# Optimization experiments

Hardware: AMD Instinct MI355X
Metric: run time of the kernel (lower is better)

Reference implementation:

```python
import jax, jax.numpy as jnp
import numpy as np

D_MODEL, D_FF, N_EXPERTS, TOP_K = 1024, 4096, 8, 2
B, S = 4, 4096


def setup_inputs() -> dict:
    key = jax.random.key(0)
    ks = jax.random.split(key, 4)
    scale_in = 1.0 / np.sqrt(D_MODEL)
    scale_ff = 1.0 / np.sqrt(D_FF)
    return {
        "x": jax.random.normal(ks[0], (B, S, D_MODEL), dtype=jnp.float32),
        "gate_w": jax.random.normal(ks[1], (D_MODEL, N_EXPERTS), dtype=jnp.float32) * scale_in,
        "gate_b": jnp.zeros((N_EXPERTS,), dtype=jnp.float32),
        "w1": jax.random.normal(ks[2], (N_EXPERTS, D_MODEL, D_FF), dtype=jnp.float32) * scale_in,
        "b1": jnp.zeros((N_EXPERTS, D_FF), dtype=jnp.float32),
        "w2": jax.random.normal(ks[3], (N_EXPERTS, D_FF, D_MODEL), dtype=jnp.float32) * scale_ff,
        "b2": jnp.zeros((N_EXPERTS, D_MODEL), dtype=jnp.float32),
    }


def reference(x, gate_w, gate_b, w1, b1, w2, b2):
    in_shape = x.shape
    tokens = x.reshape(-1, in_shape[-1])                      # [T, d]
    logits = tokens @ gate_w + gate_b                         # [T, E]
    top_w, sel = jax.lax.top_k(logits, TOP_K)                 # [T, k]
    top_w = jax.nn.softmax(top_w.astype(jnp.float32), axis=1).astype(tokens.dtype)

    out = jnp.zeros_like(tokens)
    for e in range(N_EXPERTS):
        # combined routing weight for expert e (0 if not selected) -> [T]
        coef = jnp.sum(jnp.where(sel == e, top_w, 0.0), axis=1)
        h = jax.nn.silu(tokens @ w1[e] + b1[e])               # [T, d_ff]
        y = h @ w2[e] + b2[e]                                 # [T, d]
        out = out + coef[:, None] * y
    return out.reshape(in_shape)
```

## Files before the change

kernel.cpp:

```cpp
#include <hip/hip_runtime.h>
#include <hip/hip_bf16.h>
#include <stdint.h>

#define DM 1024
#define DF 4096
#define NE 8
#define TT 16384
#define MAXTILES 144
#define CAP (MAXTILES * 256)

typedef __bf16 bf16;
typedef __attribute__((ext_vector_type(8))) __bf16 bf16x8;
typedef __attribute__((ext_vector_type(4))) __bf16 bf16x4;
typedef __attribute__((ext_vector_type(4))) float f32x4;

#define AS1 __attribute__((address_space(1)))
#define AS3 __attribute__((address_space(3)))

__device__ __forceinline__ void async16(void* lds, const void* g) {
  __builtin_amdgcn_global_load_lds((const AS1 uint32_t*)g, (AS3 uint32_t*)lds, 16, 0, 0);
}

__global__ void k_gate(const float* __restrict__ x, const float* __restrict__ gw,
                       const float* __restrict__ gb,
                       int* __restrict__ sel, float* __restrict__ cw) {
  int gid = blockIdx.x * blockDim.x + threadIdx.x;
  int tok = gid >> 6;
  int lane = threadIdx.x & 63;
  const float* xr = x + (size_t)tok * DM;
  float l[8] = {0,0,0,0,0,0,0,0};
#pragma unroll
  for (int i = 0; i < DM / 64; i++) {
    int d = i * 64 + lane;
    float xv = xr[d];
    float4 gA = *(const float4*)(gw + d * 8);
    float4 gB = *(const float4*)(gw + d * 8 + 4);
    l[0] += xv * gA.x; l[1] += xv * gA.y; l[2] += xv * gA.z; l[3] += xv * gA.w;
    l[4] += xv * gB.x; l[5] += xv * gB.y; l[6] += xv * gB.z; l[7] += xv * gB.w;
  }
#pragma unroll
  for (int e = 0; e < 8; e++) {
    float v = l[e];
    v += __shfl_xor(v, 1);  v += __shfl_xor(v, 2);  v += __shfl_xor(v, 4);
    v += __shfl_xor(v, 8);  v += __shfl_xor(v, 16); v += __shfl_xor(v, 32);
    l[e] = v + gb[e];
  }
  if (lane == 0) {
    int e0 = 0;
#pragma unroll
    for (int e = 1; e < 8; e++) if (l[e] > l[e0]) e0 = e;
    int e1 = (e0 == 0) ? 1 : 0;
#pragma unroll
    for (int e = 0; e < 8; e++) if (e != e1 && e != e0 && l[e] > l[e1]) e1 = e;
    float t = expf(l[e1] - l[e0]);
    float c0 = 1.0f / (1.0f + t);
    float c1 = t / (1.0f + t);
    sel[2 * tok] = e0;  sel[2 * tok + 1] = e1;
    cw[2 * tok] = c0;   cw[2 * tok + 1] = c1;
  }
}

__global__ void k_hist(const int* __restrict__ sel, int* __restrict__ meta) {
  __shared__ int h[8];
  if (threadIdx.x < 8) h[threadIdx.x] = 0;
  __syncthreads();
  int i = blockIdx.x * blockDim.x + threadIdx.x;
  atomicAdd(&h[sel[i]], 1);
  __syncthreads();
  if (threadIdx.x < 8) atomicAdd(&meta[threadIdx.x], h[threadIdx.x]);
}

__global__ void k_plan(int* __restrict__ meta, int* __restrict__ rows) {
  if (threadIdx.x == 0) {
    int off = 0, nt = 0;
    for (int e = 0; e < NE; e++) {
      meta[16 + e] = off;
      int c = meta[e];
      int ntile = (c + 255) >> 8;
      for (int j = 0; j < ntile; j++) {
        meta[64 + nt] = e;
        meta[64 + MAXTILES + nt] = off + j * 256;
        nt++;
      }
      off += ntile * 256;
    }
    meta[24] = nt;
    meta[25] = off;
  }
  __syncthreads();
  for (int i = threadIdx.x; i < CAP; i += blockDim.x) rows[i] = -1;
}

__global__ void k_scatter(const int* __restrict__ sel, const float* __restrict__ cw,
                          int* __restrict__ meta, int* __restrict__ rows,
                          float* __restrict__ coefs) {
  __shared__ int hcnt[8];
  __shared__ int hbase[8];
  if (threadIdx.x < 8) hcnt[threadIdx.x] = 0;
  __syncthreads();
  int slot = blockIdx.x * 256 + threadIdx.x;
  int t = slot >> 1;
  int e = sel[slot];
  int r = atomicAdd(&hcnt[e], 1);
  __syncthreads();
  if (threadIdx.x < 8) hbase[threadIdx.x] = atomicAdd(&meta[8 + threadIdx.x], hcnt[threadIdx.x]);
  __syncthreads();
  int pos = meta[16 + e] + hbase[e] + r;
  rows[pos] = t;
  coefs[pos] = cw[slot];
}

__global__ void k_gather(const float* __restrict__ x, const int* __restrict__ rows,
                         const int* __restrict__ meta, bf16* __restrict__ xg) {
  int pos = blockIdx.x;
  if (pos >= meta[25]) return;
  int t = rows[pos];
  int c = threadIdx.x * 4;
  bf16x4 o;
  if (t >= 0) {
    float4 f = *(const float4*)(x + (size_t)t * DM + c);
    o[0] = (bf16)f.x; o[1] = (bf16)f.y; o[2] = (bf16)f.z; o[3] = (bf16)f.w;
  } else {
    o[0] = (bf16)0.0f; o[1] = (bf16)0.0f; o[2] = (bf16)0.0f; o[3] = (bf16)0.0f;
  }
  *(bf16x4*)(xg + (size_t)pos * DM + c) = o;
}

__global__ void k_transcast(const float* __restrict__ src, bf16* __restrict__ dst,
                            int srcRS, size_t srcE, size_t dstE, int R) {
  __shared__ float tile[64][65];
  src += blockIdx.z * srcE;
  dst += blockIdx.z * dstE;
  int r0 = blockIdx.y * 64, c0 = blockIdx.x * 64;
  int tr = threadIdx.x >> 4;
  int tc = (threadIdx.x & 15) * 4;
#pragma unroll
  for (int i = 0; i < 4; i++) {
    int r = tr + i * 16;
    float4 f = *(const float4*)(src + (size_t)(r0 + r) * srcRS + (c0 + tc));
    tile[r][tc] = f.x; tile[r][tc + 1] = f.y; tile[r][tc + 2] = f.z; tile[r][tc + 3] = f.w;
  }
  __syncthreads();
#pragma unroll
  for (int i = 0; i < 4; i++) {
    int cc = tr + i * 16;
    bf16x4 o;
    o[0] = (bf16)tile[tc + 0][cc];
    o[1] = (bf16)tile[tc + 1][cc];
    o[2] = (bf16)tile[tc + 2][cc];
    o[3] = (bf16)tile[tc + 3][cc];
    *(bf16x4*)(dst + (size_t)(c0 + cc) * R + (r0 + tc)) = o;
  }
}

template<int MODE>
__global__ __launch_bounds__(512, 1) void k_gemm(
    const bf16* __restrict__ A, const bf16* __restrict__ Bw,
    const float* __restrict__ bias, int bstride,
    bf16* __restrict__ H, float* __restrict__ Out, int addBias,
    const int* __restrict__ rows, const float* __restrict__ coefs,
    const int* __restrict__ meta, int KT, int NT) {
  int T = meta[24];
  int ngx = NT >> 8;
  int nact = ngx * T;
  int b = blockIdx.x;
  if (b >= nact) return;
  int q = nact >> 3, rr = nact & 7;
  int xcd = b & 7, i = b >> 3;
  int j = xcd * q + (xcd < rr ? xcd : rr) + i;
  int gT4 = T << 2;
  int g = j / gT4;
  int rem = j - g * gT4;
  int tidb = rem >> 2;
  int xnb = (g << 2) + (rem & 3);
  int e = meta[64 + tidb];
  int row0 = meta[64 + MAXTILES + tidb];
  int n0 = xnb << 8;

  __shared__ __align__(16) bf16 As[2][256 * 64];
  __shared__ __align__(16) bf16 Bs[2][256 * 64];

  int t = threadIdx.x;
  int lane = t & 63;
  int w = t >> 6;
  int wm = w >> 2, wn = w & 3;

  int arow = t >> 3;
  int k8 = ((t & 7) ^ (arow & 7)) * 8;
  const bf16* Ab = A + (size_t)(row0 + arow) * KT + k8;
  const bf16* Bb = Bw + ((size_t)e * NT + n0 + arow) * KT + k8;
  size_t rstep = (size_t)64 * KT;
  int ldso = t * 8;

  f32x4 acc[8][4] = {};

  auto stage_B_A02 = [&](int kt, int buf) {
    const bf16* a = Ab + kt;
    const bf16* b2 = Bb + kt;
    bf16* la = &As[buf][ldso];
    bf16* lb = &Bs[buf][ldso];
    async16(lb,         b2);
    async16(lb + 4096,  b2 + rstep);
    async16(lb + 8192,  b2 + 2 * rstep);
    async16(lb + 12288, b2 + 3 * rstep);
    async16(la,         a);
    async16(la + 8192,  a + 2 * rstep);
  };
  auto stage_A13 = [&](int kt, int buf) {
    const bf16* a = Ab + kt;
    bf16* la = &As[buf][ldso];
    async16(la + 4096,  a + rstep);
    async16(la + 12288, a + 3 * rstep);
  };

  int rA = (wm * 128 + (lane & 15)) * 64;
  int rB = (wn * 64 + (lane & 15)) * 64;
  int kx0 = ((lane >> 4) * 8) ^ ((lane & 7) * 8);
  int kx1 = kx0 ^ 32;

  int nt = KT >> 6;
  stage_B_A02(0, 0);
  stage_A13(0, 0);
  stage_B_A02(64, 1);
  asm volatile("s_waitcnt vmcnt(8)" ::: "memory");
  __builtin_amdgcn_s_barrier();

  bf16x8 bfr[2][4];
  for (int tau = 0; tau < nt; ++tau) {
    int s = tau & 1;
    const bf16* Ap = &As[s][rA];
    const bf16* Bp = &Bs[s][rB];
    {
      bf16x8 af[2][4];
#pragma unroll
      for (int ni = 0; ni < 4; ni++) {
        bfr[0][ni] = *(const bf16x8*)&Bp[ni * 1024 + kx0];
        bfr[1][ni] = *(const bf16x8*)&Bp[ni * 1024 + kx1];
      }
#pragma unroll
      for (int mi = 0; mi < 4; mi++) {
        af[0][mi] = *(const bf16x8*)&Ap[mi * 1024 + kx0];
        af[1][mi] = *(const bf16x8*)&Ap[mi * 1024 + kx1];
      }
      if (tau + 1 < nt) stage_A13((tau + 1) << 6, s ^ 1);
      __builtin_amdgcn_s_setprio(1);
#pragma unroll
      for (int ks = 0; ks < 2; ks++)
#pragma unroll
        for (int mi = 0; mi < 4; mi++)
#pragma unroll
          for (int ni = 0; ni < 4; ni++)
            acc[mi][ni] = __builtin_amdgcn_mfma_f32_16x16x32_bf16(
                af[ks][mi], bfr[ks][ni], acc[mi][ni], 0, 0, 0);
      __builtin_amdgcn_s_setprio(0);
    }
    if (tau < nt - 1) asm volatile("s_waitcnt vmcnt(8)" ::: "memory");
    else              asm volatile("s_waitcnt vmcnt(0)" ::: "memory");
    __builtin_amdgcn_s_barrier();
    {
      bf16x8 af[2][4];
#pragma unroll
      for (int mi = 0; mi < 4; mi++) {
        af[0][mi] = *(const bf16x8*)&Ap[(mi + 4) * 1024 + kx0];
        af[1][mi] = *(const bf16x8*)&Ap[(mi + 4) * 1024 + kx1];
      }
      if (tau + 2 < nt) stage_B_A02((tau + 2) << 6, s);
      __builtin_amdgcn_s_setprio(1);
#pragma unroll
      for (int ks = 0; ks < 2; ks++)
#pragma unroll
        for (int mi = 0; mi < 4; mi++)
#pragma unroll
          for (int ni = 0; ni < 4; ni++)
            acc[mi + 4][ni] = __builtin_amdgcn_mfma_f32_16x16x32_bf16(
                af[ks][mi], bfr[ks][ni], acc[mi + 4][ni], 0, 0, 0);
      __builtin_amdgcn_s_setprio(0);
    }
    if (tau < nt - 2)       asm volatile("s_waitcnt vmcnt(8)" ::: "memory");
    else if (tau == nt - 2) asm volatile("s_waitcnt vmcnt(2)" ::: "memory");
    else                    asm volatile("s_waitcnt vmcnt(0)" ::: "memory");
    __builtin_amdgcn_s_barrier();
  }

  int rq = (lane >> 4) * 4;
  int cq = lane & 15;
  float bv[4];
#pragma unroll
  for (int ni = 0; ni < 4; ni++)
    bv[ni] = bias[e * bstride + n0 + wn * 64 + ni * 16 + cq];

  if (MODE == 0) {
#pragma unroll
    for (int mi = 0; mi < 8; mi++) {
#pragma unroll
      for (int i2 = 0; i2 < 4; i2++) {
        int gr = row0 + wm * 128 + mi * 16 + rq + i2;
        bf16* hr = H + (size_t)gr * NT + n0 + wn * 64;
#pragma unroll
        for (int ni = 0; ni < 4; ni++) {
          float v = acc[mi][ni][i2] + bv[ni];
          float sg = v / (1.0f + __expf(-v));
          hr[ni * 16 + cq] = (bf16)sg;
        }
      }
    }
  } else {
#pragma unroll
    for (int mi = 0; mi < 8; mi++) {
#pragma unroll
      for (int i2 = 0; i2 < 4; i2++) {
        int gr = row0 + wm * 128 + mi * 16 + rq + i2;
        int trow = rows[gr];
        if (trow < 0) continue;
        float cf = coefs[gr];
        float* orow = Out + (size_t)trow * DM + n0 + wn * 64;
#pragma unroll
        for (int ni = 0; ni < 4; ni++) {
          float v = acc[mi][ni][i2];
          if (addBias) v += bv[ni];
          atomicAdd(&orow[ni * 16 + cq], cf * v);
        }
      }
    }
  }
}

extern "C" void kernel_launch(void* const* d_in, const int* in_sizes, int n_in,
                              void* d_out, int out_size, void* d_ws, size_t ws_size,
                              hipStream_t stream) {
  const float* x  = (const float*)d_in[0];
  const float* gw = (const float*)d_in[1];
  const float* gb = (const float*)d_in[2];
  const float* w1 = (const float*)d_in[3];
  const float* b1 = (const float*)d_in[4];
  const float* w2 = (const float*)d_in[5];
  const float* b2 = (const float*)d_in[6];
  float* out = (float*)d_out;

  size_t smallB = (size_t)CAP * 4 * 2 + (size_t)TT * 2 * 4 * 2 + 8192 + 16 * 256;
  int nc = 8;
  for (int cand = 1; cand <= 8; cand <<= 1) {
    size_t dfc = DF / cand;
    size_t need = 2 * ((size_t)NE * dfc * DM * 2)
                + (size_t)CAP * DM * 2
                + (size_t)CAP * dfc * 2
                + smallB;
    if (need <= ws_size) { nc = cand; break; }
  }
  const int DFC = DF / nc;

  char* ws = (char*)d_ws;
  size_t off = 0;
  auto alloc = [&](size_t bytes) -> void* {
    void* p = ws + off;
    off += (bytes + 255) & ~(size_t)255;
    return p;
  };
  bf16* w1tc = (bf16*)alloc((size_t)NE * DFC * DM * 2);
  bf16* w2tc = (bf16*)alloc((size_t)NE * DM * DFC * 2);
  bf16* xg   = (bf16*)alloc((size_t)CAP * DM * 2);
  bf16* h    = (bf16*)alloc((size_t)CAP * DFC * 2);
  int* rows  = (int*)alloc((size_t)CAP * 4);
  float* cof = (float*)alloc((size_t)CAP * 4);
  int* sel   = (int*)alloc((size_t)TT * 2 * 4);
  float* cw  = (float*)alloc((size_t)TT * 2 * 4);
  int* meta  = (int*)alloc(8192);

  hipMemsetAsync(meta, 0, 256, stream);
  hipMemsetAsync(out, 0, (size_t)out_size * sizeof(float), stream);
  k_gate<<<TT / 4, 256, 0, stream>>>(x, gw, gb, sel, cw);
  k_hist<<<2 * TT / 256, 256, 0, stream>>>(sel, meta);
  k_plan<<<1, 256, 0, stream>>>(meta, rows);
  k_scatter<<<2 * TT / 256, 256, 0, stream>>>(sel, cw, meta, rows, cof);
  k_gather<<<CAP, 256, 0, stream>>>(x, rows, meta, xg);

  for (int c = 0; c < nc; c++) {
    const float* w1c = w1 + (size_t)c * DFC;
    const float* w2c = w2 + (size_t)c * DFC * DM;
    k_transcast<<<dim3(DFC / 64, DM / 64, NE), 256, 0, stream>>>(
        w1c, w1tc, DF, (size_t)DM * DF, (size_t)DFC * DM, DM);
    k_transcast<<<dim3(DM / 64, DFC / 64, NE), 256, 0, stream>>>(
        w2c, w2tc, DM, (size_t)DF * DM, (size_t)DM * DFC, DFC);
    k_gemm<0><<<(DFC / 256) * MAXTILES, 512, 0, stream>>>(
        xg, w1tc, b1 + (size_t)c * DFC, DF, h, nullptr, 0, rows, cof, meta, DM, DFC);
    k_gemm<1><<<(DM / 256) * MAXTILES, 512, 0, stream>>>(
        h, w2tc, b2, DM, nullptr, out, (c == 0) ? 1 : 0, rows, cof, meta, DFC, DM);
  }
}
```

Before: 955.1 us.

## Split each GEMM K-tile half into two phases with interleaved async loads

The main loop of the expert GEMM now processes each half of the 64-wide K tile in two 32-wide sub-phases separated by extra barriers. The global-to-LDS async loads for the next tiles are spread across these four phases instead of issued in two bursts. Only half of the fragments are held live at a time, which lowers register pressure. The goal is to smooth memory issue against MFMA work, at the cost of two extra workgroup barriers per iteration.

```diff
diff --git a/kernel.cpp b/kernel.cpp
--- a/kernel.cpp
+++ b/kernel.cpp
@@ -194,34 +194,25 @@
 
   f32x4 acc[8][4] = {};
 
-  auto stage_B_A02 = [&](int kt, int buf) {
-    const bf16* a = Ab + kt;
-    const bf16* b2 = Bb + kt;
-    bf16* la = &As[buf][ldso];
-    bf16* lb = &Bs[buf][ldso];
-    async16(lb,         b2);
-    async16(lb + 4096,  b2 + rstep);
-    async16(lb + 8192,  b2 + 2 * rstep);
-    async16(lb + 12288, b2 + 3 * rstep);
-    async16(la,         a);
-    async16(la + 8192,  a + 2 * rstep);
-  };
-  auto stage_A13 = [&](int kt, int buf) {
-    const bf16* a = Ab + kt;
-    bf16* la = &As[buf][ldso];
-    async16(la + 4096,  a + rstep);
-    async16(la + 12288, a + 3 * rstep);
-  };
-
   int rA = (wm * 128 + (lane & 15)) * 64;
   int rB = (wn * 64 + (lane & 15)) * 64;
   int kx0 = ((lane >> 4) * 8) ^ ((lane & 7) * 8);
   int kx1 = kx0 ^ 32;
 
   int nt = KT >> 6;
-  stage_B_A02(0, 0);
-  stage_A13(0, 0);
-  stage_B_A02(64, 1);
+  {
+    const bf16* a0 = Ab;  const bf16* b0 = Bb;
+    bf16* la = &As[0][ldso];  bf16* lb = &Bs[0][ldso];
+    async16(lb, b0); async16(lb + 4096, b0 + rstep);
+    async16(lb + 8192, b0 + 2 * rstep); async16(lb + 12288, b0 + 3 * rstep);
+    async16(la, a0); async16(la + 8192, a0 + 2 * rstep);
+    async16(la + 4096, a0 + rstep); async16(la + 12288, a0 + 3 * rstep);
+    const bf16* a1 = Ab + 64;  const bf16* b1 = Bb + 64;
+    bf16* la1 = &As[1][ldso];  bf16* lb1 = &Bs[1][ldso];
+    async16(lb1, b1); async16(lb1 + 4096, b1 + rstep);
+    async16(lb1 + 8192, b1 + 2 * rstep); async16(lb1 + 12288, b1 + 3 * rstep);
+    async16(la1, a1); async16(la1 + 8192, a1 + 2 * rstep);
+  }
   asm volatile("s_waitcnt vmcnt(8)" ::: "memory");
   __builtin_amdgcn_s_barrier();
 
@@ -230,50 +221,83 @@
     int s = tau & 1;
     const bf16* Ap = &As[s][rA];
     const bf16* Bp = &Bs[s][rB];
+    const bf16* An = Ab + ((tau + 1) << 6);
+    bf16* lan = &As[s ^ 1][ldso];
+    const bf16* An2 = Ab + ((tau + 2) << 6);
+    const bf16* Bn2 = Bb + ((tau + 2) << 6);
+    bf16* lan2 = &As[s][ldso];
+    bf16* lbn2 = &Bs[s][ldso];
     {
-      bf16x8 af[2][4];
-#pragma unroll
-      for (int ni = 0; ni < 4; ni++) {
-        bfr[0][ni] = *(const bf16x8*)&Bp[ni * 1024 + kx0];
-        bfr[1][ni] = *(const bf16x8*)&Bp[ni * 1024 + kx1];
-      }
-#pragma unroll
-      for (int mi = 0; mi < 4; mi++) {
-        af[0][mi] = *(const bf16x8*)&Ap[mi * 1024 + kx0];
-        af[1][mi] = *(const bf16x8*)&Ap[mi * 1024 + kx1];
-      }
-      if (tau + 1 < nt) stage_A13((tau + 1) << 6, s ^ 1);
+      bf16x8 af[4];
+#pragma unroll
+      for (int ni = 0; ni < 4; ni++) bfr[0][ni] = *(const bf16x8*)&Bp[ni * 1024 + kx0];
+#pragma unroll
+      for (int mi = 0; mi < 4; mi++) af[mi] = *(const bf16x8*)&Ap[mi * 1024 + kx0];
+      if (tau + 1 < nt) async16(lan + 4096, An + rstep);
       __builtin_amdgcn_s_setprio(1);
 #pragma unroll
-      for (int ks = 0; ks < 2; ks++)
-#pragma unroll
-        for (int mi = 0; mi < 4; mi++)
-#pragma unroll
-          for (int ni = 0; ni < 4; ni++)
-            acc[mi][ni] = __builtin_amdgcn_mfma_f32_16x16x32_bf16(
-                af[ks][mi], bfr[ks][ni], acc[mi][ni], 0, 0, 0);
+      for (int mi = 0; mi < 4; mi++)
+#pragma unroll
+        for (int ni = 0; ni < 4; ni++)
+          acc[mi][ni] = __builtin_amdgcn_mfma_f32_16x16x32_bf16(
+              af[mi], bfr[0][ni], acc[mi][ni], 0, 0, 0);
+      __builtin_amdgcn_s_setprio(0);
+    }
+    __builtin_amdgcn_s_barrier();
+    {
+      bf16x8 af[4];
+#pragma unroll
+      for (int ni = 0; ni < 4; ni++) bfr[1][ni] = *(const bf16x8*)&Bp[ni * 1024 + kx1];
+#pragma unroll
+      for (int mi = 0; mi < 4; mi++) af[mi] = *(const bf16x8*)&Ap[mi * 1024 + kx1];
+      if (tau + 1 < nt) async16(lan + 12288, An + 3 * rstep);
+      __builtin_amdgcn_s_setprio(1);
+#pragma unroll
+      for (int mi = 0; mi < 4; mi++)
+#pragma unroll
+        for (int ni = 0; ni < 4; ni++)
+          acc[mi][ni] = __builtin_amdgcn_mfma_f32_16x16x32_bf16(
+              af[mi], bfr[1][ni], acc[mi][ni], 0, 0, 0);
       __builtin_amdgcn_s_setprio(0);
     }
     if (tau < nt - 1) asm volatile("s_waitcnt vmcnt(8)" ::: "memory");
     else              asm volatile("s_waitcnt vmcnt(0)" ::: "memory");
     __builtin_amdgcn_s_barrier();
     {
-      bf16x8 af[2][4];
-#pragma unroll
-      for (int mi = 0; mi < 4; mi++) {
-        af[0][mi] = *(const bf16x8*)&Ap[(mi + 4) * 1024 + kx0];
-        af[1][mi] = *(const bf16x8*)&Ap[(mi + 4) * 1024 + kx1];
+      bf16x8 af[4];
+#pragma unroll
+      for (int mi = 0; mi < 4; mi++) af[mi] = *(const bf16x8*)&Ap[(mi + 4) * 1024 + kx0];
+      if (tau + 2 < nt) {
+        async16(lbn2, Bn2);
+        async16(lbn2 + 4096, Bn2 + rstep);
+        async16(lbn2 + 8192, Bn2 + 2 * rstep);
       }
-      if (tau + 2 < nt) stage_B_A02((tau + 2) << 6, s);
       __builtin_amdgcn_s_setprio(1);
 #pragma unroll
-      for (int ks = 0; ks < 2; ks++)
-#pragma unroll
-        for (int mi = 0; mi < 4; mi++)
-#pragma unroll
-          for (int ni = 0; ni < 4; ni++)
-            acc[mi + 4][ni] = __builtin_amdgcn_mfma_f32_16x16x32_bf16(
-                af[ks][mi], bfr[ks][ni], acc[mi + 4][ni], 0, 0, 0);
+      for (int mi = 0; mi < 4; mi++)
+#pragma unroll
+        for (int ni = 0; ni < 4; ni++)
+          acc[mi + 4][ni] = __builtin_amdgcn_mfma_f32_16x16x32_bf16(
+              af[mi], bfr[0][ni], acc[mi + 4][ni], 0, 0, 0);
+      __builtin_amdgcn_s_setprio(0);
+    }
+    __builtin_amdgcn_s_barrier();
+    {
+      bf16x8 af[4];
+#pragma unroll
+      for (int mi = 0; mi < 4; mi++) af[mi] = *(const bf16x8*)&Ap[(mi + 4) * 1024 + kx1];
+      if (tau + 2 < nt) {
+        async16(lbn2 + 12288, Bn2 + 3 * rstep);
+        async16(lan2, An2);
+        async16(lan2 + 8192, An2 + 2 * rstep);
+      }
+      __builtin_amdgcn_s_setprio(1);
+#pragma unroll
+      for (int mi = 0; mi < 4; mi++)
+#pragma unroll
+        for (int ni = 0; ni < 4; ni++)
+          acc[mi + 4][ni] = __builtin_amdgcn_mfma_f32_16x16x32_bf16(
+              af[mi], bfr[1][ni], acc[mi + 4][ni], 0, 0, 0);
       __builtin_amdgcn_s_setprio(0);
     }
     if (tau < nt - 2)       asm volatile("s_waitcnt vmcnt(8)" ::: "memory");
```

New measurement: 1.110 ms. 16.2% more time.

## Shrink MoE GEMM tiles to 128x128 with 256-thread blocks and simpler pipeline

Applied to the files above, without the earlier changes.

Reduces the grouped GEMM block tile from 256x256 (512 threads, 1 block per CU) to 128x128 (256 threads, 2 blocks per CU), and regroups expert row tiles into 128-row chunks. Smaller chunks cut padding waste per expert, and the smaller tile raises occupancy. The software pipeline is simplified to a plain double buffer with a full vmcnt(0) wait plus barrier each k-step. In exchange, each tile does less compute per byte loaded, so global and LDS traffic per FLOP roughly doubles, and pipelining is shallower.

```diff
diff --git a/kernel.cpp b/kernel.cpp
--- a/kernel.cpp
+++ b/kernel.cpp
@@ -6,8 +6,8 @@
 #define DF 4096
 #define NE 8
 #define TT 16384
-#define MAXTILES 144
-#define CAP (MAXTILES * 256)
+#define MAXTILES 264
+#define CAP (MAXTILES * 128)
 
 typedef __bf16 bf16;
 typedef __attribute__((ext_vector_type(8))) __bf16 bf16x8;
@@ -76,13 +76,13 @@
     for (int e = 0; e < NE; e++) {
       meta[16 + e] = off;
       int c = meta[e];
-      int ntile = (c + 255) >> 8;
+      int ntile = (c + 127) >> 7;
       for (int j = 0; j < ntile; j++) {
         meta[64 + nt] = e;
-        meta[64 + MAXTILES + nt] = off + j * 256;
+        meta[64 + MAXTILES + nt] = off + j * 128;
         nt++;
       }
-      off += ntile * 256;
+      off += ntile * 128;
     }
     meta[24] = nt;
     meta[25] = off;
@@ -154,14 +154,14 @@
 }
 
 template<int MODE>
-__global__ __launch_bounds__(512, 1) void k_gemm(
+__global__ __launch_bounds__(256, 2) void k_gemm(
     const bf16* __restrict__ A, const bf16* __restrict__ Bw,
     const float* __restrict__ bias, int bstride,
     bf16* __restrict__ H, float* __restrict__ Out, int addBias,
     const int* __restrict__ rows, const float* __restrict__ coefs,
     const int* __restrict__ meta, int KT, int NT) {
   int T = meta[24];
-  int ngx = NT >> 8;
+  int ngx = NT >> 7;
   int nact = ngx * T;
   int b = blockIdx.x;
   if (b >= nact) return;
@@ -175,111 +175,94 @@
   int xnb = (g << 2) + (rem & 3);
   int e = meta[64 + tidb];
   int row0 = meta[64 + MAXTILES + tidb];
-  int n0 = xnb << 8;
-
-  __shared__ __align__(16) bf16 As[2][256 * 64];
-  __shared__ __align__(16) bf16 Bs[2][256 * 64];
+  int n0 = xnb << 7;
+
+  __shared__ __align__(16) bf16 As[2][128 * 64];
+  __shared__ __align__(16) bf16 Bs[2][128 * 64];
 
   int t = threadIdx.x;
   int lane = t & 63;
   int w = t >> 6;
-  int wm = w >> 2, wn = w & 3;
-
-  int arow = t >> 3;
-  int k8 = ((t & 7) ^ (arow & 7)) * 8;
-  const bf16* Ab = A + (size_t)(row0 + arow) * KT + k8;
-  const bf16* Bb = Bw + ((size_t)e * NT + n0 + arow) * KT + k8;
-  size_t rstep = (size_t)64 * KT;
+  int wm = w >> 1, wn = w & 1;
+
+  int r0 = t >> 3;
+  int k8 = ((t & 7) ^ (r0 & 7)) * 8;
+  const bf16* Ab = A + (size_t)(row0 + r0) * KT + k8;
+  const bf16* Bb = Bw + ((size_t)e * NT + n0 + r0) * KT + k8;
+  size_t rstep = (size_t)32 * KT;
   int ldso = t * 8;
 
-  f32x4 acc[8][4] = {};
-
-  auto stage_B_A02 = [&](int kt, int buf) {
-    const bf16* a = Ab + kt;
-    const bf16* b2 = Bb + kt;
-    bf16* la = &As[buf][ldso];
-    bf16* lb = &Bs[buf][ldso];
-    async16(lb,         b2);
-    async16(lb + 4096,  b2 + rstep);
-    async16(lb + 8192,  b2 + 2 * rstep);
-    async16(lb + 12288, b2 + 3 * rstep);
-    async16(la,         a);
-    async16(la + 8192,  a + 2 * rstep);
-  };
-  auto stage_A13 = [&](int kt, int buf) {
+  f32x4 acc[4][4] = {};
+
+  auto stageA = [&](int kt, int buf) {
     const bf16* a = Ab + kt;
     bf16* la = &As[buf][ldso];
-    async16(la + 4096,  a + rstep);
-    async16(la + 12288, a + 3 * rstep);
+    async16(la,        a);
+    async16(la + 2048, a + rstep);
+    async16(la + 4096, a + 2 * rstep);
+    async16(la + 6144, a + 3 * rstep);
   };
-
-  int rA = (wm * 128 + (lane & 15)) * 64;
+  auto stageB = [&](int kt, int buf) {
+    const bf16* bb = Bb + kt;
+    bf16* lb = &Bs[buf][ldso];
+    async16(lb,        bb);
+    async16(lb + 2048, bb + rstep);
+    async16(lb + 4096, bb + 2 * rstep);
+    async16(lb + 6144, bb + 3 * rstep);
+  };
+
+  int rA = (wm * 64 + (lane & 15)) * 64;
   int rB = (wn * 64 + (lane & 15)) * 64;
   int kx0 = ((lane >> 4) * 8) ^ ((lane & 7) * 8);
   int kx1 = kx0 ^ 32;
 
   int nt = KT >> 6;
-  stage_B_A02(0, 0);
-  stage_A13(0, 0);
-  stage_B_A02(64, 1);
-  asm volatile("s_waitcnt vmcnt(8)" ::: "memory");
+  stageA(0, 0);
+  stageB(0, 0);
+  asm volatile("s_waitcnt vmcnt(0)" ::: "memory");
   __builtin_amdgcn_s_barrier();
 
-  bf16x8 bfr[2][4];
   for (int tau = 0; tau < nt; ++tau) {
     int s = tau & 1;
     const bf16* Ap = &As[s][rA];
     const bf16* Bp = &Bs[s][rB];
+    bool pre = (tau + 1 < nt);
+    if (pre) stageA((tau + 1) << 6, s ^ 1);
     {
-      bf16x8 af[2][4];
-#pragma unroll
-      for (int ni = 0; ni < 4; ni++) {
-        bfr[0][ni] = *(const bf16x8*)&Bp[ni * 1024 + kx0];
-        bfr[1][ni] = *(const bf16x8*)&Bp[ni * 1024 + kx1];
-      }
-#pragma unroll
-      for (int mi = 0; mi < 4; mi++) {
-        af[0][mi] = *(const bf16x8*)&Ap[mi * 1024 + kx0];
-        af[1][mi] = *(const bf16x8*)&Ap[mi * 1024 + kx1];
-      }
-      if (tau + 1 < nt) stage_A13((tau + 1) << 6, s ^ 1);
+      bf16x8 af[4], bfr[4];
+#pragma unroll
+      for (int ni = 0; ni < 4; ni++) bfr[ni] = *(const bf16x8*)&Bp[ni * 1024 + kx0];
+#pragma unroll
+      for (int mi = 0; mi < 4; mi++) af[mi] = *(const bf16x8*)&Ap[mi * 1024 + kx0];
       __builtin_amdgcn_s_setprio(1);
 #pragma unroll
-      for (int ks = 0; ks < 2; ks++)
-#pragma unroll
-        for (int mi = 0; mi < 4; mi++)
-#pragma unroll
-          for (int ni = 0; ni < 4; ni++)
-            acc[mi][ni] = __builtin_amdgcn_mfma_f32_16x16x32_bf16(
-                af[ks][mi], bfr[ks][ni], acc[mi][ni], 0, 0, 0);
+      for (int mi = 0; mi < 4; mi++)
+#pragma unroll
+        for (int ni = 0; ni < 4; ni++)
+          acc[mi][ni] = __builtin_amdgcn_mfma_f32_16x16x32_bf16(
+              af[mi], bfr[ni], acc[mi][ni], 0, 0, 0);
       __builtin_amdgcn_s_setprio(0);
     }
-    if (tau < nt - 1) asm volatile("s_waitcnt vmcnt(8)" ::: "memory");
-    else              asm volatile("s_waitcnt vmcnt(0)" ::: "memory");
-    __builtin_amdgcn_s_barrier();
+    if (pre) stageB((tau + 1) << 6, s ^ 1);
     {
-      bf16x8 af[2][4];
-#pragma unroll
-      for (int mi = 0; mi < 4; mi++) {
-        af[0][mi] = *(const bf16x8*)&Ap[(mi + 4) * 1024 + kx0];
-        af[1][mi] = *(const bf16x8*)&Ap[(mi + 4) * 1024 + kx1];
-      }
-      if (tau + 2 < nt) stage_B_A02((tau + 2) << 6, s);
+      bf16x8 af[4], bfr[4];
+#pragma unroll
+      for (int ni = 0; ni < 4; ni++) bfr[ni] = *(const bf16x8*)&Bp[ni * 1024 + kx1];
+#pragma unroll
+      for (int mi = 0; mi < 4; mi++) af[mi] = *(const bf16x8*)&Ap[mi * 1024 + kx1];
       __builtin_amdgcn_s_setprio(1);
 #pragma unroll
-      for (int ks = 0; ks < 2; ks++)
-#pragma unroll
-        for (int mi = 0; mi < 4; mi++)
-#pragma unroll
-          for (int ni = 0; ni < 4; ni++)
-            acc[mi + 4][ni] = __builtin_amdgcn_mfma_f32_16x16x32_bf16(
-                af[ks][mi], bfr[ks][ni], acc[mi + 4][ni], 0, 0, 0);
+      for (int mi = 0; mi < 4; mi++)
+#pragma unroll
+        for (int ni = 0; ni < 4; ni++)
+          acc[mi][ni] = __builtin_amdgcn_mfma_f32_16x16x32_bf16(
+              af[mi], bfr[ni], acc[mi][ni], 0, 0, 0);
       __builtin_amdgcn_s_setprio(0);
     }
-    if (tau < nt - 2)       asm volatile("s_waitcnt vmcnt(8)" ::: "memory");
-    else if (tau == nt - 2) asm volatile("s_waitcnt vmcnt(2)" ::: "memory");
-    else                    asm volatile("s_waitcnt vmcnt(0)" ::: "memory");
-    __builtin_amdgcn_s_barrier();
+    if (pre) {
+      asm volatile("s_waitcnt vmcnt(0)" ::: "memory");
+      __builtin_amdgcn_s_barrier();
+    }
   }
 
   int rq = (lane >> 4) * 4;
@@ -291,10 +274,10 @@
 
   if (MODE == 0) {
 #pragma unroll
-    for (int mi = 0; mi < 8; mi++) {
+    for (int mi = 0; mi < 4; mi++) {
 #pragma unroll
       for (int i2 = 0; i2 < 4; i2++) {
-        int gr = row0 + wm * 128 + mi * 16 + rq + i2;
+        int gr = row0 + wm * 64 + mi * 16 + rq + i2;
         bf16* hr = H + (size_t)gr * NT + n0 + wn * 64;
 #pragma unroll
         for (int ni = 0; ni < 4; ni++) {
@@ -306,10 +289,10 @@
     }
   } else {
 #pragma unroll
-    for (int mi = 0; mi < 8; mi++) {
+    for (int mi = 0; mi < 4; mi++) {
 #pragma unroll
       for (int i2 = 0; i2 < 4; i2++) {
-        int gr = row0 + wm * 128 + mi * 16 + rq + i2;
+        int gr = row0 + wm * 64 + mi * 16 + rq + i2;
         int trow = rows[gr];
         if (trow < 0) continue;
         float cf = coefs[gr];
@@ -381,9 +364,9 @@
         w1c, w1tc, DF, (size_t)DM * DF, (size_t)DFC * DM, DM);
     k_transcast<<<dim3(DM / 64, DFC / 64, NE), 256, 0, stream>>>(
         w2c, w2tc, DM, (size_t)DF * DM, (size_t)DM * DFC, DFC);
-    k_gemm<0><<<(DFC / 256) * MAXTILES, 512, 0, stream>>>(
+    k_gemm<0><<<(DFC / 128) * MAXTILES, 256, 0, stream>>>(
         xg, w1tc, b1 + (size_t)c * DFC, DF, h, nullptr, 0, rows, cof, meta, DM, DFC);
-    k_gemm<1><<<(DM / 256) * MAXTILES, 512, 0, stream>>>(
+    k_gemm<1><<<(DM / 128) * MAXTILES, 256, 0, stream>>>(
         h, w2tc, b2, DM, nullptr, out, (c == 0) ? 1 : 0, rows, cof, meta, DFC, DM);
   }
 }
```

After: 1.260 ms. 1.32x slower.

## Replace double-buffered split staging with single-buffer BK=128 synchronous loads

Applied to the files above, without the earlier changes.

Replaces the double-buffered LDS pipeline (64-wide K tiles, with A and B loads split and interleaved across two half-iterations) with a single 128-wide K buffer. Each tile is loaded fully, the code waits for vmcnt(0), then computes. This simplifies the schedule and halves the number of barrier rounds per K element, but global loads no longer overlap with MFMA work within a block. Any hiding of load latency must now come from other resident blocks, and occupancy is limited by the large LDS footprint.

```diff
diff --git a/kernel.cpp b/kernel.cpp
--- a/kernel.cpp
+++ b/kernel.cpp
@@ -177,109 +177,68 @@
   int row0 = meta[64 + MAXTILES + tidb];
   int n0 = xnb << 8;
 
-  __shared__ __align__(16) bf16 As[2][256 * 64];
-  __shared__ __align__(16) bf16 Bs[2][256 * 64];
+  __shared__ __align__(16) bf16 As[256 * 128];
+  __shared__ __align__(16) bf16 Bs[256 * 128];
 
   int t = threadIdx.x;
   int lane = t & 63;
   int w = t >> 6;
   int wm = w >> 2, wn = w & 3;
 
-  int arow = t >> 3;
-  int k8 = ((t & 7) ^ (arow & 7)) * 8;
+  int arow = t >> 4;
+  int k8 = ((t & 15) ^ (arow & 7)) * 8;
   const bf16* Ab = A + (size_t)(row0 + arow) * KT + k8;
   const bf16* Bb = Bw + ((size_t)e * NT + n0 + arow) * KT + k8;
-  size_t rstep = (size_t)64 * KT;
+  size_t rstep32 = (size_t)32 * KT;
   int ldso = t * 8;
 
   f32x4 acc[8][4] = {};
 
-  auto stage_B_A02 = [&](int kt, int buf) {
+  auto stage = [&](int kt) {
     const bf16* a = Ab + kt;
-    const bf16* b2 = Bb + kt;
-    bf16* la = &As[buf][ldso];
-    bf16* lb = &Bs[buf][ldso];
-    async16(lb,         b2);
-    async16(lb + 4096,  b2 + rstep);
-    async16(lb + 8192,  b2 + 2 * rstep);
-    async16(lb + 12288, b2 + 3 * rstep);
-    async16(la,         a);
-    async16(la + 8192,  a + 2 * rstep);
+    const bf16* bb = Bb + kt;
+    bf16* la = &As[ldso];
+    bf16* lb = &Bs[ldso];
+#pragma unroll
+    for (int i2 = 0; i2 < 8; i2++) async16(la + i2 * 4096, a + i2 * rstep32);
+#pragma unroll
+    for (int i2 = 0; i2 < 8; i2++) async16(lb + i2 * 4096, bb + i2 * rstep32);
   };
-  auto stage_A13 = [&](int kt, int buf) {
-    const bf16* a = Ab + kt;
-    bf16* la = &As[buf][ldso];
-    async16(la + 4096,  a + rstep);
-    async16(la + 12288, a + 3 * rstep);
-  };
-
-  int rA = (wm * 128 + (lane & 15)) * 64;
-  int rB = (wn * 64 + (lane & 15)) * 64;
-  int kx0 = ((lane >> 4) * 8) ^ ((lane & 7) * 8);
-  int kx1 = kx0 ^ 32;
-
-  int nt = KT >> 6;
-  stage_B_A02(0, 0);
-  stage_A13(0, 0);
-  stage_B_A02(64, 1);
-  asm volatile("s_waitcnt vmcnt(8)" ::: "memory");
+
+  int rA = (wm * 128 + (lane & 15)) * 128;
+  int rB = (wn * 64 + (lane & 15)) * 128;
+
+  int nt = KT >> 7;
+  stage(0);
+  asm volatile("s_waitcnt vmcnt(0)" ::: "memory");
   __builtin_amdgcn_s_barrier();
 
-  bf16x8 bfr[2][4];
   for (int tau = 0; tau < nt; ++tau) {
-    int s = tau & 1;
-    const bf16* Ap = &As[s][rA];
-    const bf16* Bp = &Bs[s][rB];
-    {
-      bf16x8 af[2][4];
-#pragma unroll
-      for (int ni = 0; ni < 4; ni++) {
-        bfr[0][ni] = *(const bf16x8*)&Bp[ni * 1024 + kx0];
-        bfr[1][ni] = *(const bf16x8*)&Bp[ni * 1024 + kx1];
-      }
-#pragma unroll
-      for (int mi = 0; mi < 4; mi++) {
-        af[0][mi] = *(const bf16x8*)&Ap[mi * 1024 + kx0];
-        af[1][mi] = *(const bf16x8*)&Ap[mi * 1024 + kx1];
-      }
-      if (tau + 1 < nt) stage_A13((tau + 1) << 6, s ^ 1);
+    const bf16* Ap = &As[rA];
+    const bf16* Bp = &Bs[rB];
+#pragma unroll
+    for (int ks = 0; ks < 4; ks++) {
+      int kx = ((ks * 4 + (lane >> 4)) ^ (lane & 7)) * 8;
+      bf16x8 bfr[4], af[8];
+#pragma unroll
+      for (int ni = 0; ni < 4; ni++) bfr[ni] = *(const bf16x8*)&Bp[ni * 2048 + kx];
+#pragma unroll
+      for (int mi = 0; mi < 8; mi++) af[mi] = *(const bf16x8*)&Ap[mi * 2048 + kx];
       __builtin_amdgcn_s_setprio(1);
 #pragma unroll
-      for (int ks = 0; ks < 2; ks++)
-#pragma unroll
-        for (int mi = 0; mi < 4; mi++)
-#pragma unroll
-          for (int ni = 0; ni < 4; ni++)
-            acc[mi][ni] = __builtin_amdgcn_mfma_f32_16x16x32_bf16(
-                af[ks][mi], bfr[ks][ni], acc[mi][ni], 0, 0, 0);
+      for (int mi = 0; mi < 8; mi++)
+#pragma unroll
+        for (int ni = 0; ni < 4; ni++)
+          acc[mi][ni] = __builtin_amdgcn_mfma_f32_16x16x32_bf16(
+              af[mi], bfr[ni], acc[mi][ni], 0, 0, 0);
       __builtin_amdgcn_s_setprio(0);
     }
-    if (tau < nt - 1) asm volatile("s_waitcnt vmcnt(8)" ::: "memory");
-    else              asm volatile("s_waitcnt vmcnt(0)" ::: "memory");
-    __builtin_amdgcn_s_barrier();
-    {
-      bf16x8 af[2][4];
-#pragma unroll
-      for (int mi = 0; mi < 4; mi++) {
-        af[0][mi] = *(const bf16x8*)&Ap[(mi + 4) * 1024 + kx0];
-        af[1][mi] = *(const bf16x8*)&Ap[(mi + 4) * 1024 + kx1];
-      }
-      if (tau + 2 < nt) stage_B_A02((tau + 2) << 6, s);
-      __builtin_amdgcn_s_setprio(1);
-#pragma unroll
-      for (int ks = 0; ks < 2; ks++)
-#pragma unroll
-        for (int mi = 0; mi < 4; mi++)
-#pragma unroll
-          for (int ni = 0; ni < 4; ni++)
-            acc[mi + 4][ni] = __builtin_amdgcn_mfma_f32_16x16x32_bf16(
-                af[ks][mi], bfr[ks][ni], acc[mi + 4][ni], 0, 0, 0);
-      __builtin_amdgcn_s_setprio(0);
-    }
-    if (tau < nt - 2)       asm volatile("s_waitcnt vmcnt(8)" ::: "memory");
-    else if (tau == nt - 2) asm volatile("s_waitcnt vmcnt(2)" ::: "memory");
-    else                    asm volatile("s_waitcnt vmcnt(0)" ::: "memory");
-    __builtin_amdgcn_s_barrier();
+    if (tau + 1 < nt) {
+      __builtin_amdgcn_s_barrier();
+      stage((tau + 1) << 7);
+      asm volatile("s_waitcnt vmcnt(0)" ::: "memory");
+      __builtin_amdgcn_s_barrier();
+    }
   }
 
   int rq = (lane >> 4) * 4;
```

Result: slower. 1.144 ms (+19.7%).
